# Kernel tuning notes

Hardware: AMD Instinct MI355X
Metric: run time of the kernel (lower is better)

## Reference

```python
import jax, jax.numpy as jnp
import numpy as np

HEADS = 4
DIM_HEAD = 64
SCALE = DIM_HEAD ** -0.5


def setup_inputs() -> dict:
    key = jax.random.key(0)
    k1, k2, k3 = jax.random.split(key, 3)
    C = 256
    hidden = HEADS * DIM_HEAD  # 256
    x = jax.random.normal(k1, (16, C, 64, 64), dtype=jnp.float32)
    # 1x1 conv weights collapsed to [out, in] matrices
    w_qkv = jax.random.normal(k2, (3 * hidden, C), dtype=jnp.float32) * (C ** -0.5)
    w_out = jax.random.normal(k3, (C, hidden), dtype=jnp.float32) * (hidden ** -0.5)
    b_out = jnp.zeros((C,), dtype=jnp.float32)
    return {"x": x, "w_qkv": w_qkv, "w_out": w_out, "b_out": b_out}


def reference(x, w_qkv, w_out, b_out):
    b, c, h, w = x.shape
    n = h * w
    # 1x1 conv == channel GEMM
    qkv = jnp.einsum('bchw,oc->bohw', x, w_qkv)           # [b, 3*hidden, h, w]
    qkv = qkv.reshape(b, 3, HEADS, DIM_HEAD, n)            # [b, 3, H, d, n]
    q, k, v = qkv[:, 0], qkv[:, 1], qkv[:, 2]              # each [b, H, d, n]
    q = jax.nn.softmax(q, axis=2) * SCALE                  # softmax over d
    k = jax.nn.softmax(k, axis=3)                          # softmax over n
    context = jnp.einsum('bhdn,bhen->bhde', k, v)          # [b, H, d, e]
    out = jnp.einsum('bhde,bhdn->bhen', context, q)        # [b, H, e, n]
    out = out.reshape(b, HEADS * DIM_HEAD, h, w)           # [b, hidden, h, w]
    return jnp.einsum('bchw,oc->bohw', out, w_out) + b_out[None, :, None, None]
```

## Files before the change

### kernel.cpp

```cpp
#include <hip/hip_runtime.h>

#define NPIX 4096
#define SCALE 0.125f

typedef _Float16 half8 __attribute__((ext_vector_type(8)));
typedef _Float16 half4 __attribute__((ext_vector_type(4)));
typedef float floatx4 __attribute__((ext_vector_type(4)));

__device__ __forceinline__ void async16(void* lds, const void* g) {
  __builtin_amdgcn_global_load_lds(
      (const __attribute__((address_space(1))) unsigned int*)(uintptr_t)g,
      (__attribute__((address_space(3))) unsigned int*)(unsigned)(uintptr_t)lds,
      16, 0, 0);
}

__device__ __forceinline__ void vmwait(int n) {
  if (n >= 6)      asm volatile("s_waitcnt vmcnt(6)" ::: "memory");
  else if (n >= 4) asm volatile("s_waitcnt vmcnt(4)" ::: "memory");
  else             asm volatile("s_waitcnt vmcnt(0)" ::: "memory");
}

__device__ __forceinline__ void pipe_barrier(int n) {
  __builtin_amdgcn_sched_barrier(0);
  vmwait(n);
  __builtin_amdgcn_s_barrier();
  __builtin_amdgcn_sched_barrier(0);
}

__global__ __launch_bounds__(256) void split16_kernel(const float* __restrict__ w,
                                                      _Float16* __restrict__ hi,
                                                      _Float16* __restrict__ lo, int n) {
  int i = blockIdx.x * 256 + threadIdx.x;
  if (i < n) {
    float v = w[i];
    _Float16 h = (_Float16)v;
    hi[i] = h;
    lo[i] = (_Float16)(v - (float)h);
  }
}

__global__ __launch_bounds__(256) void transpose16_kernel(const float* __restrict__ x,
                                                          _Float16* __restrict__ xt) {
  __shared__ float t[64][65];
  const int n0 = blockIdx.x * 64, c0 = blockIdx.y * 64, b = blockIdx.z;
  const float* xp = x + (long)b * 256 * NPIX;
  const int tid = threadIdx.x;
  const int r = tid >> 4, c4 = (tid & 15) * 4;
#pragma unroll
  for (int p = 0; p < 4; p++) {
    float4 v = *(const float4*)&xp[(long)(c0 + r + p * 16) * NPIX + n0 + c4];
    t[r + p * 16][c4 + 0] = v.x;
    t[r + p * 16][c4 + 1] = v.y;
    t[r + p * 16][c4 + 2] = v.z;
    t[r + p * 16][c4 + 3] = v.w;
  }
  __syncthreads();
  const int n = tid >> 2, cg = (tid & 3) * 16;
  alignas(16) _Float16 o[16];
#pragma unroll
  for (int i = 0; i < 16; i++) o[i] = (_Float16)t[cg + i][n];
  _Float16* dst = &xt[((long)b * NPIX + n0 + n) * 256 + c0 + cg];
  *(float4*)dst = *(float4*)&o[0];
  *(float4*)(dst + 8) = *(float4*)&o[8];
}

#define CPB 2
__global__ __launch_bounds__(256) void kv_ctx_gemm(const _Float16* __restrict__ Ahp,
                                                   const _Float16* __restrict__ Bt,
                                                   float* __restrict__ pbuf,
                                                   float* __restrict__ rsbuf) {
  union alignas(16) KVU {
    _Float16 st[3][2][128 * 32];
    _Float16 ev[128][136];
  };
  __shared__ KVU u;
  const int tid = threadIdx.x;
  const int cg = blockIdx.x;
  const int hi = blockIdx.y;
  const int b = blockIdx.z;
  const _Float16* Bp = Bt + (long)b * NPIX * 256;
  const int wv = tid >> 6, l = tid & 63;
  const int r16 = l & 15, q = l >> 4;
  const int mb = (wv >> 1) * 64, nb = (wv & 1) * 64;
  const int r1 = tid >> 2;
  const int o1 = ((tid & 3) * 8) ^ (((r1 >> 1) & 3) * 8);
  const int ldsc1 = (wv * 64) * 8;
  const int ldsc2 = (256 + wv * 64) * 8;
  const int q8 = (q * 8) ^ (((r16 >> 1) & 3) * 8);
  const long gAk = (long)(256 + hi * 64 + r1) * 256;
  const long gAv = (long)(512 + hi * 64 + r1) * 256;

  auto STAGE = [&](int buf, int kt, int n0) {
    const int k0 = kt * 32;
    async16(&u.st[buf][0][ldsc1], &Ahp[gAk + k0 + o1]);
    async16(&u.st[buf][0][ldsc2], &Ahp[gAv + k0 + o1]);
    async16(&u.st[buf][1][ldsc1], &Bp[(long)(n0 + r1) * 256 + k0 + o1]);
    async16(&u.st[buf][1][ldsc2], &Bp[(long)(n0 + 64 + r1) * 256 + k0 + o1]);
  };

  floatx4 c2[4];
#pragma unroll
  for (int j = 0; j < 4; j++) c2[j] = (floatx4){0.f, 0.f, 0.f, 0.f};
  float rs = 0.f;

  for (int cs = 0; cs < CPB; cs++) {
    const int n0 = (cg * CPB + cs) * 128;
    floatx4 acc[4][4];
#pragma unroll
    for (int i = 0; i < 4; i++)
#pragma unroll
      for (int j = 0; j < 4; j++) acc[i][j] = (floatx4){0.f, 0.f, 0.f, 0.f};

    STAGE(0, 0, n0);
    STAGE(1, 1, n0);
    pipe_barrier(4);
    int cc = 0;
    for (int kt = 0; kt < 8; kt++) {
      if (kt < 6) {
        int sb = cc + 2;
        if (sb >= 3) sb -= 3;
        STAGE(sb, kt + 2, n0);
      }
      half8 fa[4], fb[4];
#pragma unroll
      for (int i = 0; i < 4; i++) {
        fa[i] = *(const half8*)&u.st[cc][0][(mb + i * 16 + r16) * 32 + q8];
        fb[i] = *(const half8*)&u.st[cc][1][(nb + i * 16 + r16) * 32 + q8];
      }
#pragma unroll
      for (int i = 0; i < 4; i++)
#pragma unroll
        for (int j = 0; j < 4; j++)
          acc[i][j] = __builtin_amdgcn_mfma_f32_16x16x32_f16(fa[i], fb[j], acc[i][j], 0, 0, 0);
      pipe_barrier(kt < 6 ? 4 : 0);
      cc = (cc == 2) ? 0 : cc + 1;
    }

    const bool is_k = (mb == 0);
#pragma unroll
    for (int i = 0; i < 4; i++) {
      const int row = mb + i * 16 + q * 4;
#pragma unroll
      for (int j = 0; j < 4; j++) {
        const int col = nb + j * 16 + r16;
#pragma unroll
        for (int t = 0; t < 4; t++) {
          const float vv0 = acc[i][j][t];
          u.ev[row + t][col] = (_Float16)(is_k ? __expf(vv0) : vv0);
        }
      }
    }
    __syncthreads();

#pragma unroll
    for (int ks = 0; ks < 4; ks++) {
      half8 a = *(const half8*)&u.ev[wv * 16 + r16][ks * 32 + q * 8];
#pragma unroll
      for (int ii = 0; ii < 8; ii++) rs += (float)a[ii];
#pragma unroll
      for (int j = 0; j < 4; j++) {
        half8 bv = *(const half8*)&u.ev[64 + j * 16 + r16][ks * 32 + q * 8];
        c2[j] = __builtin_amdgcn_mfma_f32_16x16x32_f16(a, bv, c2[j], 0, 0, 0);
      }
    }
    __syncthreads();
  }

  rs += __shfl_xor(rs, 16, 64);
  rs += __shfl_xor(rs, 32, 64);
  const int bh = b * 4 + hi;
  float* pp = pbuf + ((long)bh * 16 + cg) * 4096;
#pragma unroll
  for (int j = 0; j < 4; j++)
#pragma unroll
    for (int reg = 0; reg < 4; reg++)
      pp[(wv * 16 + q * 4 + reg) * 64 + j * 16 + r16] = c2[j][reg];
  if (l < 16) rsbuf[((long)bh * 16 + cg) * 64 + wv * 16 + r16] = rs;
}

__global__ __launch_bounds__(256) void mctx_fused(const float* __restrict__ w_out,
                                                  const float* __restrict__ pbuf,
                                                  const float* __restrict__ rsbuf,
                                                  _Float16* __restrict__ Mhi,
                                                  _Float16* __restrict__ Mlo) {
  __shared__ float sctxT[64][65];
  __shared__ float sinv[64];
  const int cq = blockIdx.x, h = blockIdx.y, b = blockIdx.z;
  const int bh = b * 4 + h;
  const float* pp = pbuf + (long)bh * 16 * 4096;
  const int tid = threadIdx.x;
  {
    const int d = tid >> 2, e0 = (tid & 3) * 16;
    float s0[16];
#pragma unroll
    for (int i = 0; i < 16; i++) s0[i] = 0.f;
    for (int c = 0; c < 16; c++) {
#pragma unroll
      for (int k = 0; k < 4; k++) {
        float4 v = *(const float4*)&pp[(long)c * 4096 + d * 64 + e0 + k * 4];
        s0[k * 4 + 0] += v.x;
        s0[k * 4 + 1] += v.y;
        s0[k * 4 + 2] += v.z;
        s0[k * 4 + 3] += v.w;
      }
    }
#pragma unroll
    for (int i = 0; i < 16; i++) sctxT[e0 + i][d] = s0[i];
  }
  if (tid < 64) {
    const float* rp = rsbuf + (long)bh * 16 * 64 + tid;
    float z = 0.f;
#pragma unroll
    for (int c = 0; c < 16; c++) z += rp[c * 64];
    sinv[tid] = 1.0f / z;
  }
  __syncthreads();
  const int c = cq * 64 + (tid >> 2);
  const int d0 = (tid & 3) * 16;
  const float* wp = w_out + (long)c * 256 + h * 64;
  float acc[16];
#pragma unroll
  for (int i = 0; i < 16; i++) acc[i] = 0.f;
#pragma unroll
  for (int e4 = 0; e4 < 16; e4++) {
    float4 wv = *(const float4*)&wp[e4 * 4];
#pragma unroll
    for (int u2 = 0; u2 < 4; u2++) {
      const float we = ((const float*)&wv)[u2];
      const int e = e4 * 4 + u2;
#pragma unroll
      for (int dd = 0; dd < 16; dd++) acc[dd] = fmaf(we, sctxT[e][d0 + dd], acc[dd]);
    }
  }
  alignas(16) _Float16 hi16[16], lo16[16];
#pragma unroll
  for (int k4 = 0; k4 < 4; k4++) {
    float4 zv = *(const float4*)&sinv[d0 + k4 * 4];
#pragma unroll
    for (int u2 = 0; u2 < 4; u2++) {
      const int dd = k4 * 4 + u2;
      float v = acc[dd] * (SCALE * ((const float*)&zv)[u2]);
      _Float16 hh = (_Float16)v;
      hi16[dd] = hh;
      lo16[dd] = (_Float16)(v - (float)hh);
    }
  }
  _Float16* mh = Mhi + ((long)b * 256 + c) * 256 + h * 64 + d0;
  _Float16* ml = Mlo + ((long)b * 256 + c) * 256 + h * 64 + d0;
#pragma unroll
  for (int k = 0; k < 2; k++) {
    *(float4*)&mh[k * 8] = *(float4*)&hi16[k * 8];
    *(float4*)&ml[k * 8] = *(float4*)&lo16[k * 8];
  }
}

__global__ __launch_bounds__(512) void qout_fused(const _Float16* __restrict__ wqh,
                                                  const _Float16* __restrict__ wql,
                                                  const _Float16* __restrict__ xt,
                                                  const _Float16* __restrict__ Mhi,
                                                  const _Float16* __restrict__ Mlo,
                                                  const float* __restrict__ bias,
                                                  float* __restrict__ out) {
  struct alignas(16) QO {
    _Float16 st[2][20480];
    _Float16 P[128][256];
  };
  __shared__ QO u;
  const int tid = threadIdx.x;
  const int n0 = blockIdx.x * 128;
  const int b = blockIdx.y;
  const _Float16* Bp = xt + (long)b * NPIX * 256;
  const _Float16* MhB = Mhi + (long)b * 65536;
  const _Float16* MlB = Mlo + (long)b * 65536;
  float* Cp = out + (long)b * 256 * NPIX;
  const int wv = tid >> 6, l = tid & 63;
  const int r16 = l & 15, q = l >> 4;
  const int mb = (wv >> 1) * 64;
  const int nb = (wv & 1) * 64;
  const int r1 = tid >> 2;
  const int o1 = ((tid & 3) * 8) ^ (((r1 >> 1) & 3) * 8);
  const int ldsW = wv * 512;
  const int q8 = (q * 8) ^ (((r16 >> 1) & 3) * 8);

  auto STAGE1 = [&](int buf, int kt) {
    const int k0 = kt * 32;
    async16(&u.st[buf][0 + ldsW], &wqh[(long)r1 * 256 + k0 + o1]);
    async16(&u.st[buf][4096 + ldsW], &wqh[(long)(128 + r1) * 256 + k0 + o1]);
    async16(&u.st[buf][8192 + ldsW], &wql[(long)r1 * 256 + k0 + o1]);
    async16(&u.st[buf][12288 + ldsW], &wql[(long)(128 + r1) * 256 + k0 + o1]);
    async16(&u.st[buf][16384 + ldsW], &Bp[(long)(n0 + r1) * 256 + k0 + o1]);
  };
  auto STAGE2 = [&](int buf, int kt) {
    const int k0 = kt * 32;
    async16(&u.st[buf][0 + ldsW], &MhB[(long)r1 * 256 + k0 + o1]);
    async16(&u.st[buf][4096 + ldsW], &MhB[(long)(128 + r1) * 256 + k0 + o1]);
    async16(&u.st[buf][8192 + ldsW], &MlB[(long)r1 * 256 + k0 + o1]);
    async16(&u.st[buf][12288 + ldsW], &MlB[(long)(128 + r1) * 256 + k0 + o1]);
  };

  floatx4 acc[4][4];
#pragma unroll
  for (int i = 0; i < 4; i++)
#pragma unroll
    for (int j = 0; j < 4; j++) acc[i][j] = (floatx4){0.f, 0.f, 0.f, 0.f};

  STAGE1(0, 0);
  __syncthreads();
  for (int kt = 0; kt < 8; kt++) {
    const int cur = kt & 1;
    if (kt < 7) STAGE1(cur ^ 1, kt + 1);
    half8 fa[4], flo[4], fb[4];
#pragma unroll
    for (int i = 0; i < 4; i++) {
      fa[i] = *(const half8*)&u.st[cur][(mb + i * 16 + r16) * 32 + q8];
      flo[i] = *(const half8*)&u.st[cur][8192 + (mb + i * 16 + r16) * 32 + q8];
      fb[i] = *(const half8*)&u.st[cur][16384 + (nb + i * 16 + r16) * 32 + q8];
    }
#pragma unroll
    for (int i = 0; i < 4; i++)
#pragma unroll
      for (int j = 0; j < 4; j++) {
        acc[i][j] = __builtin_amdgcn_mfma_f32_16x16x32_f16(fa[i], fb[j], acc[i][j], 0, 0, 0);
        acc[i][j] = __builtin_amdgcn_mfma_f32_16x16x32_f16(flo[i], fb[j], acc[i][j], 0, 0, 0);
      }
    __syncthreads();
  }

  STAGE2(0, 0);

#pragma unroll
  for (int j = 0; j < 4; j++) {
    float s = 0.f;
#pragma unroll
    for (int i = 0; i < 4; i++)
#pragma unroll
      for (int t = 0; t < 4; t++) {
        float e = __expf(acc[i][j][t]);
        acc[i][j][t] = e;
        s += e;
      }
    s += __shfl_xor(s, 16, 64);
    s += __shfl_xor(s, 32, 64);
    const float rinv = 1.0f / s;
    const int nl = nb + j * 16 + r16;
    const int swz = (nl & 7) * 8;
#pragma unroll
    for (int i = 0; i < 4; i++) {
      half4 h4;
#pragma unroll
      for (int t = 0; t < 4; t++) h4[t] = (_Float16)(acc[i][j][t] * rinv);
      *(half4*)&u.P[nl][(mb + i * 16 + q * 4) ^ swz] = h4;
    }
  }
  __syncthreads();

  floatx4 ac2[4][4];
#pragma unroll
  for (int i = 0; i < 4; i++)
#pragma unroll
    for (int j = 0; j < 4; j++) ac2[i][j] = (floatx4){0.f, 0.f, 0.f, 0.f};

  for (int kt = 0; kt < 8; kt++) {
    const int cur = kt & 1;
    if (kt < 7) STAGE2(cur ^ 1, kt + 1);
    half8 fa[4], flo[4], fb[4];
#pragma unroll
    for (int i = 0; i < 4; i++) {
      fa[i] = *(const half8*)&u.st[cur][(mb + i * 16 + r16) * 32 + q8];
      flo[i] = *(const half8*)&u.st[cur][8192 + (mb + i * 16 + r16) * 32 + q8];
      const int nrow = nb + i * 16 + r16;
      fb[i] = *(const half8*)&u.P[nrow][(kt * 32 + q * 8) ^ ((nrow & 7) * 8)];
    }
#pragma unroll
    for (int i = 0; i < 4; i++)
#pragma unroll
      for (int j = 0; j < 4; j++) {
        ac2[i][j] = __builtin_amdgcn_mfma_f32_16x16x32_f16(fa[i], fb[j], ac2[i][j], 0, 0, 0);
        ac2[i][j] = __builtin_amdgcn_mfma_f32_16x16x32_f16(flo[i], fb[j], ac2[i][j], 0, 0, 0);
      }
    __syncthreads();
  }

#pragma unroll
  for (int i = 0; i < 4; i++) {
    const int mrow = mb + i * 16 + q * 4;
#pragma unroll
    for (int t = 0; t < 4; t++) {
      float bz = bias[mrow + t];
#pragma unroll
      for (int j = 0; j < 4; j++) {
        Cp[(long)(mrow + t) * NPIX + n0 + nb + j * 16 + r16] = ac2[i][j][t] + bz;
      }
    }
  }
}

extern "C" void kernel_launch(void* const* d_in, const int* in_sizes, int n_in,
                              void* d_out, int out_size, void* d_ws, size_t ws_size,
                              hipStream_t stream) {
  const float* x = (const float*)d_in[0];
  const float* w_qkv = (const float*)d_in[1];
  const float* w_out = (const float*)d_in[2];
  const float* b_out = (const float*)d_in[3];
  float* out = (float*)d_out;

  _Float16* xt = (_Float16*)d_ws;
  float* pbuf = (float*)(xt + (long)16 * NPIX * 256);
  float* rsbuf = pbuf + (long)64 * 16 * 4096;
  _Float16* wq_hi = (_Float16*)(rsbuf + 64 * 16 * 64);
  _Float16* wq_lo = wq_hi + 768 * 256;
  _Float16* Mhi = wq_lo + 768 * 256;
  _Float16* Mlo = Mhi + 16 * 256 * 256;

  split16_kernel<<<768, 256, 0, stream>>>(w_qkv, wq_hi, wq_lo, 768 * 256);
  transpose16_kernel<<<dim3(64, 4, 16), 256, 0, stream>>>(x, xt);
  kv_ctx_gemm<<<dim3(16, 4, 16), 256, 0, stream>>>(wq_hi, xt, pbuf, rsbuf);
  mctx_fused<<<dim3(4, 4, 16), 256, 0, stream>>>(w_out, pbuf, rsbuf, Mhi, Mlo);
  qout_fused<<<dim3(32, 16), 512, 0, stream>>>(wq_hi, wq_lo, xt, Mhi, Mlo, b_out, out);
}
```

Measured before the change: 200.8 us.

## Fuse weight split into transpose kernel and read A operands directly from global

Merges the weight hi/lo split kernel into the transpose kernel as an extra z-slice, removing one launch. In qout_fused, the A operands (Wq hi/lo and M hi/lo) are no longer staged through LDS. Each wave loads its fragments straight from global/L2, which cuts LDS usage and removes the second loop's barriers. The cost is uncoalesced, unpipelined global fragment loads inside the MFMA loops, which may stall on memory latency.

```diff
diff --git a/kernel.cpp b/kernel.cpp
--- a/kernel.cpp
+++ b/kernel.cpp
@@ -27,24 +27,27 @@
   __builtin_amdgcn_sched_barrier(0);
 }
 
-__global__ __launch_bounds__(256) void split16_kernel(const float* __restrict__ w,
-                                                      _Float16* __restrict__ hi,
-                                                      _Float16* __restrict__ lo, int n) {
-  int i = blockIdx.x * 256 + threadIdx.x;
-  if (i < n) {
-    float v = w[i];
-    _Float16 h = (_Float16)v;
-    hi[i] = h;
-    lo[i] = (_Float16)(v - (float)h);
-  }
-}
-
-__global__ __launch_bounds__(256) void transpose16_kernel(const float* __restrict__ x,
-                                                          _Float16* __restrict__ xt) {
+__global__ __launch_bounds__(256) void prep_kernel(const float* __restrict__ x,
+                                                   _Float16* __restrict__ xt,
+                                                   const float* __restrict__ w_qkv,
+                                                   _Float16* __restrict__ wq_hi,
+                                                   _Float16* __restrict__ wq_lo) {
+  const int tid = threadIdx.x;
+  if (blockIdx.z == 16) {
+    int base = (blockIdx.x * 4 + blockIdx.y) * 256 + tid;
+#pragma unroll
+    for (int r = 0; r < 3; r++) {
+      int i = base + r * 65536;
+      float v = w_qkv[i];
+      _Float16 h = (_Float16)v;
+      wq_hi[i] = h;
+      wq_lo[i] = (_Float16)(v - (float)h);
+    }
+    return;
+  }
   __shared__ float t[64][65];
   const int n0 = blockIdx.x * 64, c0 = blockIdx.y * 64, b = blockIdx.z;
   const float* xp = x + (long)b * 256 * NPIX;
-  const int tid = threadIdx.x;
   const int r = tid >> 4, c4 = (tid & 15) * 4;
 #pragma unroll
   for (int p = 0; p < 4; p++) {
@@ -262,7 +265,7 @@
                                                   const float* __restrict__ bias,
                                                   float* __restrict__ out) {
   struct alignas(16) QO {
-    _Float16 st[2][20480];
+    _Float16 Bst[2][128 * 32];
     _Float16 P[128][256];
   };
   __shared__ QO u;
@@ -279,24 +282,11 @@
   const int nb = (wv & 1) * 64;
   const int r1 = tid >> 2;
   const int o1 = ((tid & 3) * 8) ^ (((r1 >> 1) & 3) * 8);
-  const int ldsW = wv * 512;
   const int q8 = (q * 8) ^ (((r16 >> 1) & 3) * 8);
 
-  auto STAGE1 = [&](int buf, int kt) {
-    const int k0 = kt * 32;
-    async16(&u.st[buf][0 + ldsW], &wqh[(long)r1 * 256 + k0 + o1]);
-    async16(&u.st[buf][4096 + ldsW], &wqh[(long)(128 + r1) * 256 + k0 + o1]);
-    async16(&u.st[buf][8192 + ldsW], &wql[(long)r1 * 256 + k0 + o1]);
-    async16(&u.st[buf][12288 + ldsW], &wql[(long)(128 + r1) * 256 + k0 + o1]);
-    async16(&u.st[buf][16384 + ldsW], &Bp[(long)(n0 + r1) * 256 + k0 + o1]);
+  auto STAGE_B = [&](int buf, int kt) {
+    async16(&u.Bst[buf][wv * 512], &Bp[(long)(n0 + r1) * 256 + kt * 32 + o1]);
   };
-  auto STAGE2 = [&](int buf, int kt) {
-    const int k0 = kt * 32;
-    async16(&u.st[buf][0 + ldsW], &MhB[(long)r1 * 256 + k0 + o1]);
-    async16(&u.st[buf][4096 + ldsW], &MhB[(long)(128 + r1) * 256 + k0 + o1]);
-    async16(&u.st[buf][8192 + ldsW], &MlB[(long)r1 * 256 + k0 + o1]);
-    async16(&u.st[buf][12288 + ldsW], &MlB[(long)(128 + r1) * 256 + k0 + o1]);
-  };
 
   floatx4 acc[4][4];
 #pragma unroll
@@ -304,17 +294,19 @@
 #pragma unroll
     for (int j = 0; j < 4; j++) acc[i][j] = (floatx4){0.f, 0.f, 0.f, 0.f};
 
-  STAGE1(0, 0);
+  STAGE_B(0, 0);
   __syncthreads();
   for (int kt = 0; kt < 8; kt++) {
     const int cur = kt & 1;
-    if (kt < 7) STAGE1(cur ^ 1, kt + 1);
+    if (kt < 7) STAGE_B(cur ^ 1, kt + 1);
+    const long ka = kt * 32 + q * 8;
     half8 fa[4], flo[4], fb[4];
 #pragma unroll
     for (int i = 0; i < 4; i++) {
-      fa[i] = *(const half8*)&u.st[cur][(mb + i * 16 + r16) * 32 + q8];
-      flo[i] = *(const half8*)&u.st[cur][8192 + (mb + i * 16 + r16) * 32 + q8];
-      fb[i] = *(const half8*)&u.st[cur][16384 + (nb + i * 16 + r16) * 32 + q8];
+      const long arow = (long)(mb + i * 16 + r16) * 256;
+      fa[i] = *(const half8*)&wqh[arow + ka];
+      flo[i] = *(const half8*)&wql[arow + ka];
+      fb[i] = *(const half8*)&u.Bst[cur][(nb + i * 16 + r16) * 32 + q8];
     }
 #pragma unroll
     for (int i = 0; i < 4; i++)
@@ -325,8 +317,6 @@
       }
     __syncthreads();
   }
-
-  STAGE2(0, 0);
 
 #pragma unroll
   for (int j = 0; j < 4; j++) {
@@ -361,15 +351,15 @@
     for (int j = 0; j < 4; j++) ac2[i][j] = (floatx4){0.f, 0.f, 0.f, 0.f};
 
   for (int kt = 0; kt < 8; kt++) {
-    const int cur = kt & 1;
-    if (kt < 7) STAGE2(cur ^ 1, kt + 1);
+    const int kc = kt * 32 + q * 8;
     half8 fa[4], flo[4], fb[4];
 #pragma unroll
     for (int i = 0; i < 4; i++) {
-      fa[i] = *(const half8*)&u.st[cur][(mb + i * 16 + r16) * 32 + q8];
-      flo[i] = *(const half8*)&u.st[cur][8192 + (mb + i * 16 + r16) * 32 + q8];
+      const long arow = (long)(mb + i * 16 + r16) * 256;
+      fa[i] = *(const half8*)&MhB[arow + kc];
+      flo[i] = *(const half8*)&MlB[arow + kc];
       const int nrow = nb + i * 16 + r16;
-      fb[i] = *(const half8*)&u.P[nrow][(kt * 32 + q * 8) ^ ((nrow & 7) * 8)];
+      fb[i] = *(const half8*)&u.P[nrow][kc ^ ((nrow & 7) * 8)];
     }
 #pragma unroll
     for (int i = 0; i < 4; i++)
@@ -378,7 +368,6 @@
         ac2[i][j] = __builtin_amdgcn_mfma_f32_16x16x32_f16(fa[i], fb[j], ac2[i][j], 0, 0, 0);
         ac2[i][j] = __builtin_amdgcn_mfma_f32_16x16x32_f16(flo[i], fb[j], ac2[i][j], 0, 0, 0);
       }
-    __syncthreads();
   }
 
 #pragma unroll
@@ -412,8 +401,7 @@
   _Float16* Mhi = wq_lo + 768 * 256;
   _Float16* Mlo = Mhi + 16 * 256 * 256;
 
-  split16_kernel<<<768, 256, 0, stream>>>(w_qkv, wq_hi, wq_lo, 768 * 256);
-  transpose16_kernel<<<dim3(64, 4, 16), 256, 0, stream>>>(x, xt);
+  prep_kernel<<<dim3(64, 4, 17), 256, 0, stream>>>(x, xt, w_qkv, wq_hi, wq_lo);
   kv_ctx_gemm<<<dim3(16, 4, 16), 256, 0, stream>>>(wq_hi, xt, pbuf, rsbuf);
   mctx_fused<<<dim3(4, 4, 16), 256, 0, stream>>>(w_out, pbuf, rsbuf, Mhi, Mlo);
   qout_fused<<<dim3(32, 16), 512, 0, stream>>>(wq_hi, wq_lo, xt, Mhi, Mlo, b_out, out);
```

Result: slower. 231.3 us (+15.2%).
